# Kernel optimization log

Hardware: AMD Instinct MI355X
Metric: run time of the kernel (lower is better)

The kernel has to match this reference:

```python
import jax, jax.numpy as jnp
import numpy as np

EPS = 1e-8
TOPK = 32

def _l2norm(x, axis=-1):
    return x / (jnp.linalg.norm(x, axis=axis, keepdims=True) + EPS)

def setup_inputs() -> dict:
    key = jax.random.key(0)
    ks = jax.random.split(key, 8)
    B, T, D, V = 16, 1024, 896, 151936
    time_feat = jax.random.normal(ks[0], (B, T, D), dtype=jnp.float32)
    text_feat = jax.random.normal(ks[1], (B, T, D), dtype=jnp.float32)
    word = jax.random.normal(ks[2], (V, D), dtype=jnp.float32)
    # nn.Linear params: W is [out_features, in_features]
    gate_w = jax.random.normal(ks[3], (D, 2 * D), dtype=jnp.float32) * (1.0 / np.sqrt(2 * D))
    gate_b = jnp.zeros((D,), dtype=jnp.float32)
    out_w = jax.random.normal(ks[4], (D, D), dtype=jnp.float32) * (1.0 / np.sqrt(D))
    out_b = jnp.zeros((D,), dtype=jnp.float32)
    return {"time_feat": time_feat, "text_feat": text_feat, "word": word,
            "gate_w": gate_w, "gate_b": gate_b, "out_w": out_w, "out_b": out_b, "s": 0}

def reference(time_feat, text_feat, word, gate_w, gate_b, out_w, out_b, s):
    # time_feat, text_feat: [B,T,D]; word: [V,D]; s is unused (as in original).
    time_mean = time_feat.mean(axis=1)                      # [B,D]
    word_norm = _l2norm(word, axis=1)                       # [V,D]
    time_norm = _l2norm(time_mean, axis=1)                  # [B,D]
    sim = jnp.einsum('bd,vd->bv', time_norm, word_norm)     # [B,V]
    _, topk_idx = jax.lax.top_k(sim, TOPK)                  # [B,K]
    selected = word[topk_idx]                               # [B,K,D] gather
    enhanced = selected.mean(axis=1)[:, None, :]            # [B,1,D]
    # softmax over singleton axis 1 -> all ones (faithful to original)
    enhanced = jax.nn.softmax(enhanced, axis=1)
    enhanced_align = text_feat * enhanced                   # [B,T,D]
    combined = jnp.concatenate([time_feat, enhanced_align], axis=-1)  # [B,T,2D]
    gate = jax.nn.sigmoid(jnp.einsum('btk,dk->btd', combined, gate_w) + gate_b)
    fused = gate * time_feat + (1.0 - gate) * text_feat
    return jnp.einsum('btd,od->bto', fused, out_w) + out_b
```

## Files before the change

kernel.cpp:

```cpp
#include <hip/hip_runtime.h>
#include <hip/hip_bf16.h>

#define D_   896
#define M_   16384
#define K1_  1792

typedef __bf16 bf16x8 __attribute__((ext_vector_type(8)));
typedef float  f32x4  __attribute__((ext_vector_type(4)));

#define GLOAD_LDS16(g, l)                                                        \
    __builtin_amdgcn_global_load_lds(                                            \
        (const __attribute__((address_space(1))) void*)(g),                      \
        (__attribute__((address_space(3))) void*)(l), 16, 0, 0)

__global__ void k_detect(const unsigned short* __restrict__ u, int* __restrict__ flag) {
    __shared__ int s;
    const int tid = threadIdx.x;
    if (tid == 0) s = 0;
    __syncthreads();
    int bad = 0;
#pragma unroll
    for (int i = 0; i < 16; ++i) {
        unsigned short v = u[(tid * 16 + i) * 2];
        int e = (v >> 7) & 0xFF;
        bad |= (e >= 0x84);
    }
    if (bad) atomicOr(&s, 1);
    __syncthreads();
    if (tid == 0) flag[0] = s;
}

__device__ inline void cvt_f32(const void* src, __hip_bfloat16* dst,
                               long long n8, long long gid, long long stride) {
    const f32x4* s = (const f32x4*)src;
    for (long long i = gid; i < n8; i += stride) {
        f32x4 a = s[2 * i], b = s[2 * i + 1];
        bf16x8 v;
#pragma unroll
        for (int t = 0; t < 4; ++t) { v[t] = (__bf16)a[t]; v[4 + t] = (__bf16)b[t]; }
        ((bf16x8*)dst)[i] = v;
    }
}
__device__ inline void cpy_bf(const void* src, __hip_bfloat16* dst,
                              long long n8, long long gid, long long stride) {
    const bf16x8* s = (const bf16x8*)src;
    for (long long i = gid; i < n8; i += stride)
        ((bf16x8*)dst)[i] = s[i];
}

__global__ __launch_bounds__(256) void k_convert(
    const void* __restrict__ tf, const void* __restrict__ xf,
    const void* __restrict__ gw, const void* __restrict__ ow,
    const void* __restrict__ gb, const void* __restrict__ ob,
    __hip_bfloat16* __restrict__ tfb, __hip_bfloat16* __restrict__ xfb,
    __hip_bfloat16* __restrict__ gwb, __hip_bfloat16* __restrict__ owb,
    float* __restrict__ gbf, float* __restrict__ obf,
    const int* __restrict__ flag)
{
    const long long gid    = (long long)blockIdx.x * 256 + threadIdx.x;
    const long long stride = (long long)gridDim.x * 256;
    const long long nTF = (long long)M_ * D_ / 8;
    const long long nGW = (long long)D_ * K1_ / 8;
    const long long nOW = (long long)D_ * D_ / 8;

    if (flag[0]) {
        cvt_f32(tf, tfb, nTF, gid, stride);
        cvt_f32(xf, xfb, nTF, gid, stride);
        cvt_f32(gw, gwb, nGW, gid, stride);
        cvt_f32(ow, owb, nOW, gid, stride);
        for (long long i = gid; i < D_; i += stride) {
            gbf[i] = ((const float*)gb)[i];
            obf[i] = ((const float*)ob)[i];
        }
    } else {
        cpy_bf(tf, tfb, nTF, gid, stride);
        cpy_bf(xf, xfb, nTF, gid, stride);
        cpy_bf(gw, gwb, nGW, gid, stride);
        cpy_bf(ow, owb, nOW, gid, stride);
        for (long long i = gid; i < D_; i += stride) {
            gbf[i] = (float)((const __hip_bfloat16*)gb)[i];
            obf[i] = (float)((const __hip_bfloat16*)ob)[i];
        }
    }
}

__global__ __launch_bounds__(256) void k_gate(
    const __hip_bfloat16* __restrict__ tfb, const __hip_bfloat16* __restrict__ xfb,
    const __hip_bfloat16* __restrict__ gwb, const float* __restrict__ gbf,
    __hip_bfloat16* __restrict__ fo)
{
    __shared__ __hip_bfloat16 As[128 * 64];
    __shared__ __hip_bfloat16 Bs[128 * 64];

    const int tid  = threadIdx.x;
    const int wid  = tid >> 6;
    const int lane = tid & 63;
    const int qm   = lane & 15;
    const int quad = lane >> 4;
    const int wm   = (wid & 1) * 64;
    const int wn   = (wid >> 1) * 64;
    const int m0   = blockIdx.x * 128;
    const int n0   = blockIdx.y * 128;
    const int arow = lane >> 3;
    const int acol = (lane & 7) * 8;

    f32x4 acc[4][4];
#pragma unroll
    for (int i = 0; i < 4; ++i)
#pragma unroll
        for (int j = 0; j < 4; ++j) acc[i][j] = (f32x4){0.f, 0.f, 0.f, 0.f};

    for (int k0 = 0; k0 < K1_; k0 += 64) {
        const __hip_bfloat16* Ab = (k0 < D_) ? (tfb + k0) : (xfb + (k0 - D_));
#pragma unroll
        for (int p = 0; p < 4; ++p) {
            const int c = p * 4 + wid;
            GLOAD_LDS16(Ab + (m0 + c * 8 + arow) * D_ + acol, As + c * 512);
            GLOAD_LDS16(gwb + (n0 + c * 8 + arow) * K1_ + k0 + acol, Bs + c * 512);
        }
        __syncthreads();
#pragma unroll
        for (int kk = 0; kk < 64; kk += 32) {
            bf16x8 a[4], b[4];
#pragma unroll
            for (int i = 0; i < 4; ++i)
                a[i] = *(const bf16x8*)(As + (wm + i * 16 + qm) * 64 + kk + quad * 8);
#pragma unroll
            for (int j = 0; j < 4; ++j)
                b[j] = *(const bf16x8*)(Bs + (wn + j * 16 + qm) * 64 + kk + quad * 8);
#pragma unroll
            for (int i = 0; i < 4; ++i)
#pragma unroll
                for (int j = 0; j < 4; ++j)
                    acc[i][j] = __builtin_amdgcn_mfma_f32_16x16x32_bf16(
                        a[i], b[j], acc[i][j], 0, 0, 0);
        }
        __syncthreads();
    }

#pragma unroll
    for (int j = 0; j < 4; ++j) {
        const int n = n0 + wn + j * 16 + qm;
        const float gbn = gbf[n];
#pragma unroll
        for (int i = 0; i < 4; ++i) {
            const int mb = m0 + wm + i * 16 + quad * 4;
#pragma unroll
            for (int r = 0; r < 4; ++r) {
                const int m = mb + r;
                const float x = acc[i][j][r] + gbn;
                const float g = 1.f / (1.f + __expf(-x));
                const float tv = (float)tfb[m * D_ + n];
                const float xv = (float)xfb[m * D_ + n];
                fo[m * D_ + n] = (__hip_bfloat16)(g * tv + (1.f - g) * xv);
            }
        }
    }
}

__global__ __launch_bounds__(256) void k_out(
    const __hip_bfloat16* __restrict__ fi,
    const __hip_bfloat16* __restrict__ owb, const float* __restrict__ obf,
    void* __restrict__ outv, const int* __restrict__ flag)
{
    __shared__ __hip_bfloat16 As[128 * 64];
    __shared__ __hip_bfloat16 Bs[128 * 64];

    const int tid  = threadIdx.x;
    const int wid  = tid >> 6;
    const int lane = tid & 63;
    const int qm   = lane & 15;
    const int quad = lane >> 4;
    const int wm   = (wid & 1) * 64;
    const int wn   = (wid >> 1) * 64;
    const int m0   = blockIdx.x * 128;
    const int n0   = blockIdx.y * 128;
    const int arow = lane >> 3;
    const int acol = (lane & 7) * 8;
    const int f32o = flag[0];

    f32x4 acc[4][4];
#pragma unroll
    for (int i = 0; i < 4; ++i)
#pragma unroll
        for (int j = 0; j < 4; ++j) acc[i][j] = (f32x4){0.f, 0.f, 0.f, 0.f};

    for (int k0 = 0; k0 < D_; k0 += 64) {
#pragma unroll
        for (int p = 0; p < 4; ++p) {
            const int c = p * 4 + wid;
            GLOAD_LDS16(fi  + (m0 + c * 8 + arow) * D_ + k0 + acol, As + c * 512);
            GLOAD_LDS16(owb + (n0 + c * 8 + arow) * D_ + k0 + acol, Bs + c * 512);
        }
        __syncthreads();
#pragma unroll
        for (int kk = 0; kk < 64; kk += 32) {
            bf16x8 a[4], b[4];
#pragma unroll
            for (int i = 0; i < 4; ++i)
                a[i] = *(const bf16x8*)(As + (wm + i * 16 + qm) * 64 + kk + quad * 8);
#pragma unroll
            for (int j = 0; j < 4; ++j)
                b[j] = *(const bf16x8*)(Bs + (wn + j * 16 + qm) * 64 + kk + quad * 8);
#pragma unroll
            for (int i = 0; i < 4; ++i)
#pragma unroll
                for (int j = 0; j < 4; ++j)
                    acc[i][j] = __builtin_amdgcn_mfma_f32_16x16x32_bf16(
                        a[i], b[j], acc[i][j], 0, 0, 0);
        }
        __syncthreads();
    }

#pragma unroll
    for (int j = 0; j < 4; ++j) {
        const int n = n0 + wn + j * 16 + qm;
        const float obn = obf[n];
#pragma unroll
        for (int i = 0; i < 4; ++i) {
            const int mb = m0 + wm + i * 16 + quad * 4;
#pragma unroll
            for (int r = 0; r < 4; ++r) {
                const int m = mb + r;
                const float v = acc[i][j][r] + obn;
                if (f32o) ((float*)outv)[m * D_ + n] = v;
                else      ((__hip_bfloat16*)outv)[m * D_ + n] = (__hip_bfloat16)v;
            }
        }
    }
}

extern "C" void kernel_launch(void* const* d_in, const int* in_sizes, int n_in,
                              void* d_out, int out_size, void* d_ws, size_t ws_size,
                              hipStream_t stream) {
    const void* tf = d_in[0];
    const void* xf = d_in[1];
    const void* gw = d_in[3];
    const void* gb = d_in[4];
    const void* ow = d_in[5];
    const void* ob = d_in[6];

    char* ws = (char*)d_ws;
    int* flag = (int*)ws;
    __hip_bfloat16* tfb   = (__hip_bfloat16*)(ws + 256);
    __hip_bfloat16* xfb   = tfb + (size_t)M_ * D_;
    __hip_bfloat16* gwb   = xfb + (size_t)M_ * D_;
    __hip_bfloat16* owb   = gwb + (size_t)D_ * K1_;
    __hip_bfloat16* fused = owb + (size_t)D_ * D_;
    float*          gbf   = (float*)(fused + (size_t)M_ * D_);
    float*          obf   = gbf + D_;

    k_detect<<<1, 256, 0, stream>>>((const unsigned short*)tf, flag);
    k_convert<<<2048, 256, 0, stream>>>(tf, xf, gw, ow, gb, ob,
                                        tfb, xfb, gwb, owb, gbf, obf, flag);

    dim3 grid(M_ / 128, D_ / 128);
    k_gate<<<grid, 256, 0, stream>>>(tfb, xfb, gwb, gbf, fused);
    k_out<<<grid, 256, 0, stream>>>(fused, owb, obf, d_out, flag);
}
```

Before: 886.2 us.

## Stage GEMM epilogues through LDS for vectorized stores; inline dtype detection

Both GEMM kernels now write their accumulators into an LDS tile reused from the operand buffers. Each thread then reads a contiguous row segment, so the epilogue loads tf/xf and stores outputs as 16-byte vectors instead of strided scalar accesses. The separate detect kernel launch is removed: each wave detects the input dtype with a ballot over sampled values, inside the convert and output kernels. The epilogue costs extra LDS traffic and syncs, and every wave redoes a small detection read.

Result: faster. 865.2 us (-2.4%).

```diff
diff --git a/kernel.cpp b/kernel.cpp
--- a/kernel.cpp
+++ b/kernel.cpp
@@ -13,21 +13,15 @@
         (const __attribute__((address_space(1))) void*)(g),                      \
         (__attribute__((address_space(3))) void*)(l), 16, 0, 0)
 
-__global__ void k_detect(const unsigned short* __restrict__ u, int* __restrict__ flag) {
-    __shared__ int s;
-    const int tid = threadIdx.x;
-    if (tid == 0) s = 0;
-    __syncthreads();
+__device__ __forceinline__ int detect_f32(const unsigned short* __restrict__ u) {
+    const int lane = threadIdx.x & 63;
     int bad = 0;
 #pragma unroll
-    for (int i = 0; i < 16; ++i) {
-        unsigned short v = u[(tid * 16 + i) * 2];
-        int e = (v >> 7) & 0xFF;
-        bad |= (e >= 0x84);
-    }
-    if (bad) atomicOr(&s, 1);
-    __syncthreads();
-    if (tid == 0) flag[0] = s;
+    for (int i = 0; i < 8; ++i) {
+        unsigned short v = u[(lane * 8 + i) * 2];
+        bad |= (((v >> 7) & 0xFF) >= 0x84);
+    }
+    return __ballot(bad) != 0ull;
 }
 
 __device__ inline void cvt_f32(const void* src, __hip_bfloat16* dst,
@@ -54,8 +48,7 @@
     const void* __restrict__ gb, const void* __restrict__ ob,
     __hip_bfloat16* __restrict__ tfb, __hip_bfloat16* __restrict__ xfb,
     __hip_bfloat16* __restrict__ gwb, __hip_bfloat16* __restrict__ owb,
-    float* __restrict__ gbf, float* __restrict__ obf,
-    const int* __restrict__ flag)
+    float* __restrict__ gbf, float* __restrict__ obf)
 {
     const long long gid    = (long long)blockIdx.x * 256 + threadIdx.x;
     const long long stride = (long long)gridDim.x * 256;
@@ -63,7 +56,7 @@
     const long long nGW = (long long)D_ * K1_ / 8;
     const long long nOW = (long long)D_ * D_ / 8;
 
-    if (flag[0]) {
+    if (detect_f32((const unsigned short*)tf)) {
         cvt_f32(tf, tfb, nTF, gid, stride);
         cvt_f32(xf, xfb, nTF, gid, stride);
         cvt_f32(gw, gwb, nGW, gid, stride);
@@ -89,8 +82,10 @@
     const __hip_bfloat16* __restrict__ gwb, const float* __restrict__ gbf,
     __hip_bfloat16* __restrict__ fo)
 {
-    __shared__ __hip_bfloat16 As[128 * 64];
-    __shared__ __hip_bfloat16 Bs[128 * 64];
+    __shared__ f32x4 smemv[128 * 66 / 4];
+    __hip_bfloat16* As = (__hip_bfloat16*)smemv;
+    __hip_bfloat16* Bs = (__hip_bfloat16*)smemv + 128 * 64;
+    float* Ts = (float*)smemv;
 
     const int tid  = threadIdx.x;
     const int wid  = tid >> 6;
@@ -98,7 +93,6 @@
     const int qm   = lane & 15;
     const int quad = lane >> 4;
     const int wm   = (wid & 1) * 64;
-    const int wn   = (wid >> 1) * 64;
     const int m0   = blockIdx.x * 128;
     const int n0   = blockIdx.y * 128;
     const int arow = lane >> 3;
@@ -127,7 +121,7 @@
                 a[i] = *(const bf16x8*)(As + (wm + i * 16 + qm) * 64 + kk + quad * 8);
 #pragma unroll
             for (int j = 0; j < 4; ++j)
-                b[j] = *(const bf16x8*)(Bs + (wn + j * 16 + qm) * 64 + kk + quad * 8);
+                b[j] = *(const bf16x8*)(Bs + (((wid >> 1) * 64) + j * 16 + qm) * 64 + kk + quad * 8);
 #pragma unroll
             for (int i = 0; i < 4; ++i)
 #pragma unroll
@@ -138,22 +132,40 @@
         __syncthreads();
     }
 
-#pragma unroll
-    for (int j = 0; j < 4; ++j) {
-        const int n = n0 + wn + j * 16 + qm;
-        const float gbn = gbf[n];
-#pragma unroll
-        for (int i = 0; i < 4; ++i) {
-            const int mb = m0 + wm + i * 16 + quad * 4;
-#pragma unroll
-            for (int r = 0; r < 4; ++r) {
-                const int m = mb + r;
-                const float x = acc[i][j][r] + gbn;
+    const int col_l = (wid >> 1) * 32 + qm;
+#pragma unroll
+    for (int ch = 0; ch < 2; ++ch) {
+        __syncthreads();
+#pragma unroll
+        for (int jj = 0; jj < 2; ++jj) {
+            const int j = ch * 2 + jj;
+            const int l = col_l + jj * 16;
+#pragma unroll
+            for (int i = 0; i < 4; ++i) {
+                const int row = wm + i * 16 + quad * 4;
+#pragma unroll
+                for (int r = 0; r < 4; ++r)
+                    Ts[(row + r) * 66 + l] = acc[i][j][r];
+            }
+        }
+        __syncthreads();
+        const int row  = tid >> 1;
+        const int half = tid & 1;
+        const size_t m = (size_t)(m0 + row);
+        const int nb   = n0 + half * 64 + ch * 32;
+        const float* tr = Ts + row * 66 + half * 32;
+#pragma unroll
+        for (int c8 = 0; c8 < 4; ++c8) {
+            bf16x8 tv = *(const bf16x8*)(tfb + m * D_ + nb + c8 * 8);
+            bf16x8 xv = *(const bf16x8*)(xfb + m * D_ + nb + c8 * 8);
+            bf16x8 ov;
+#pragma unroll
+            for (int t = 0; t < 8; ++t) {
+                const float x = tr[c8 * 8 + t] + gbf[nb + c8 * 8 + t];
                 const float g = 1.f / (1.f + __expf(-x));
-                const float tv = (float)tfb[m * D_ + n];
-                const float xv = (float)xfb[m * D_ + n];
-                fo[m * D_ + n] = (__hip_bfloat16)(g * tv + (1.f - g) * xv);
-            }
+                ov[t] = (__bf16)(g * (float)tv[t] + (1.f - g) * (float)xv[t]);
+            }
+            *(bf16x8*)(fo + m * D_ + nb + c8 * 8) = ov;
         }
     }
 }
@@ -161,10 +173,12 @@
 __global__ __launch_bounds__(256) void k_out(
     const __hip_bfloat16* __restrict__ fi,
     const __hip_bfloat16* __restrict__ owb, const float* __restrict__ obf,
-    void* __restrict__ outv, const int* __restrict__ flag)
+    void* __restrict__ outv, const unsigned short* __restrict__ tfdet)
 {
-    __shared__ __hip_bfloat16 As[128 * 64];
-    __shared__ __hip_bfloat16 Bs[128 * 64];
+    __shared__ f32x4 smemv[128 * 66 / 4];
+    __hip_bfloat16* As = (__hip_bfloat16*)smemv;
+    __hip_bfloat16* Bs = (__hip_bfloat16*)smemv + 128 * 64;
+    float* Ts = (float*)smemv;
 
     const int tid  = threadIdx.x;
     const int wid  = tid >> 6;
@@ -172,12 +186,11 @@
     const int qm   = lane & 15;
     const int quad = lane >> 4;
     const int wm   = (wid & 1) * 64;
-    const int wn   = (wid >> 1) * 64;
     const int m0   = blockIdx.x * 128;
     const int n0   = blockIdx.y * 128;
     const int arow = lane >> 3;
     const int acol = (lane & 7) * 8;
-    const int f32o = flag[0];
+    const int f32o = detect_f32(tfdet);
 
     f32x4 acc[4][4];
 #pragma unroll
@@ -201,7 +214,7 @@
                 a[i] = *(const bf16x8*)(As + (wm + i * 16 + qm) * 64 + kk + quad * 8);
 #pragma unroll
             for (int j = 0; j < 4; ++j)
-                b[j] = *(const bf16x8*)(Bs + (wn + j * 16 + qm) * 64 + kk + quad * 8);
+                b[j] = *(const bf16x8*)(Bs + (((wid >> 1) * 64) + j * 16 + qm) * 64 + kk + quad * 8);
 #pragma unroll
             for (int i = 0; i < 4; ++i)
 #pragma unroll
@@ -212,19 +225,47 @@
         __syncthreads();
     }
 
-#pragma unroll
-    for (int j = 0; j < 4; ++j) {
-        const int n = n0 + wn + j * 16 + qm;
-        const float obn = obf[n];
-#pragma unroll
-        for (int i = 0; i < 4; ++i) {
-            const int mb = m0 + wm + i * 16 + quad * 4;
-#pragma unroll
-            for (int r = 0; r < 4; ++r) {
-                const int m = mb + r;
-                const float v = acc[i][j][r] + obn;
-                if (f32o) ((float*)outv)[m * D_ + n] = v;
-                else      ((__hip_bfloat16*)outv)[m * D_ + n] = (__hip_bfloat16)v;
+    const int col_l = (wid >> 1) * 32 + qm;
+#pragma unroll
+    for (int ch = 0; ch < 2; ++ch) {
+        __syncthreads();
+#pragma unroll
+        for (int jj = 0; jj < 2; ++jj) {
+            const int j = ch * 2 + jj;
+            const int l = col_l + jj * 16;
+#pragma unroll
+            for (int i = 0; i < 4; ++i) {
+                const int row = wm + i * 16 + quad * 4;
+#pragma unroll
+                for (int r = 0; r < 4; ++r)
+                    Ts[(row + r) * 66 + l] = acc[i][j][r];
+            }
+        }
+        __syncthreads();
+        const int row  = tid >> 1;
+        const int half = tid & 1;
+        const size_t m = (size_t)(m0 + row);
+        const int nb   = n0 + half * 64 + ch * 32;
+        const float* tr = Ts + row * 66 + half * 32;
+        if (f32o) {
+            float* op = (float*)outv + m * D_ + nb;
+#pragma unroll
+            for (int c4 = 0; c4 < 8; ++c4) {
+                f32x4 w;
+#pragma unroll
+                for (int t = 0; t < 4; ++t)
+                    w[t] = tr[c4 * 4 + t] + obf[nb + c4 * 4 + t];
+                *(f32x4*)(op + c4 * 4) = w;
+            }
+        } else {
+            __hip_bfloat16* op = (__hip_bfloat16*)outv + m * D_ + nb;
+#pragma unroll
+            for (int c8 = 0; c8 < 4; ++c8) {
+                bf16x8 w;
+#pragma unroll
+                for (int t = 0; t < 8; ++t)
+                    w[t] = (__bf16)(tr[c8 * 8 + t] + obf[nb + c8 * 8 + t]);
+                *(bf16x8*)(op + c8 * 8) = w;
             }
         }
     }
@@ -241,7 +282,6 @@
     const void* ob = d_in[6];
 
     char* ws = (char*)d_ws;
-    int* flag = (int*)ws;
     __hip_bfloat16* tfb   = (__hip_bfloat16*)(ws + 256);
     __hip_bfloat16* xfb   = tfb + (size_t)M_ * D_;
     __hip_bfloat16* gwb   = xfb + (size_t)M_ * D_;
@@ -250,11 +290,11 @@
     float*          gbf   = (float*)(fused + (size_t)M_ * D_);
     float*          obf   = gbf + D_;
 
-    k_detect<<<1, 256, 0, stream>>>((const unsigned short*)tf, flag);
     k_convert<<<2048, 256, 0, stream>>>(tf, xf, gw, ow, gb, ob,
-                                        tfb, xfb, gwb, owb, gbf, obf, flag);
+                                        tfb, xfb, gwb, owb, gbf, obf);
 
     dim3 grid(M_ / 128, D_ / 128);
     k_gate<<<grid, 256, 0, stream>>>(tfb, xfb, gwb, gbf, fused);
-    k_out<<<grid, 256, 0, stream>>>(fused, owb, obf, d_out, flag);
-}
+    k_out<<<grid, 256, 0, stream>>>(fused, owb, obf, d_out,
+                                    (const unsigned short*)tf);
+}
```
